# Kernel optimization log

Measured on AMD Instinct MI355X. Metric: run time of the kernel, lower is better.

The kernel has to match this reference:

```python
import jax, jax.numpy as jnp
import numpy as np

N, E, D_IN, H, L = 50000, 800000, 256, 128, 6


def setup_inputs() -> dict:
    key = jax.random.key(0)
    ks = jax.random.split(key, 16)
    s = 0.05
    return {
        "x": jax.random.normal(ks[0], (N, D_IN), jnp.float32),
        "edge_index": jax.random.randint(ks[1], (2, E), 0, N, jnp.int32),
        "y": jax.random.randint(ks[2], (N,), 0, L, jnp.int32),
        # input projection (stored [in, out])
        "lin_w": jax.random.normal(ks[3], (D_IN, H), jnp.float32) * s,
        "lin_b": jnp.zeros((H,), jnp.float32),
        # GatedGraphConv 1: message weight [H,H], GRUCell params (torch layout [3H,H])
        "w1": jax.random.normal(ks[4], (H, H), jnp.float32) * s,
        "wih1": jax.random.normal(ks[5], (3 * H, H), jnp.float32) * s,
        "whh1": jax.random.normal(ks[6], (3 * H, H), jnp.float32) * s,
        "bih1": jnp.zeros((3 * H,), jnp.float32),
        "bhh1": jnp.zeros((3 * H,), jnp.float32),
        # GatedGraphConv 2
        "w2": jax.random.normal(ks[7], (H, H), jnp.float32) * s,
        "wih2": jax.random.normal(ks[8], (3 * H, H), jnp.float32) * s,
        "whh2": jax.random.normal(ks[9], (3 * H, H), jnp.float32) * s,
        "bih2": jnp.zeros((3 * H,), jnp.float32),
        "bhh2": jnp.zeros((3 * H,), jnp.float32),
        # classifier
        "cls_w": jax.random.normal(ks[10], (H, L), jnp.float32) * s,
        "cls_b": jnp.zeros((L,), jnp.float32),
    }


def _gated_conv(h, src, dst, w, wih, whh, bih, bhh):
    # PyG GatedGraphConv, num_layers=1: m = h @ W; aggregate add src->dst; GRUCell(m_agg, h)
    m = h @ w                                   # [N,H]
    agg = jax.ops.segment_sum(m[src], dst, num_segments=N)  # scatter-add [N,H]
    gi = agg @ wih.T + bih                      # [N,3H]
    gh = h @ whh.T + bhh                        # [N,3H]
    i_r, i_z, i_n = jnp.split(gi, 3, axis=-1)
    h_r, h_z, h_n = jnp.split(gh, 3, axis=-1)
    r = jax.nn.sigmoid(i_r + h_r)
    z = jax.nn.sigmoid(i_z + h_z)
    n = jnp.tanh(i_n + r * h_n)
    return (1.0 - z) * n + z * h


def reference(x, edge_index, y, lin_w, lin_b, w1, wih1, whh1, bih1, bhh1,
              w2, wih2, whh2, bih2, bhh2, cls_w, cls_b):
    src, dst = edge_index[0], edge_index[1]
    h = x @ lin_w + lin_b                       # [N,H]
    h = _gated_conv(h, src, dst, w1, wih1, whh1, bih1, bhh1)
    h = jax.nn.elu(h)
    h = _gated_conv(h, src, dst, w2, wih2, whh2, bih2, bhh2)
    features = h
    output = h @ cls_w + cls_b                  # [N,L]
    logp = jax.nn.log_softmax(output, axis=-1)
    loss = -jnp.mean(jnp.take_along_axis(logp, y[:, None], axis=-1))
    return output, loss, features
```

## Files before the change

### kernel.cpp

```cpp
#include <hip/hip_runtime.h>
#include <cstddef>
#include <cstdint>

typedef __attribute__((ext_vector_type(8))) short bf16x8;
typedef __attribute__((ext_vector_type(4))) float f32x4;
typedef __attribute__((ext_vector_type(8))) unsigned short u16x8;

__device__ inline unsigned short f2bf(float f) {
    unsigned u = __builtin_bit_cast(unsigned, f);
    u += 0x7FFF + ((u >> 16) & 1);
    return (unsigned short)(u >> 16);
}
__device__ inline float bfbits_lo(unsigned v) { return __builtin_bit_cast(float, v << 16); }
__device__ inline float bfbits_hi(unsigned v) { return __builtin_bit_cast(float, v & 0xffff0000u); }
__device__ inline float bf2f(unsigned short b) { return __builtin_bit_cast(float, (unsigned)b << 16); }

__device__ inline float fsigmoid(float x) { return 1.0f / (1.0f + __expf(-x)); }
__device__ inline float ftanh(float x)    { return 1.0f - 2.0f / (__expf(2.0f * x) + 1.0f); }

__device__ inline int swzB(int row, int slot) {
    return row * 64 + ((slot ^ ((row >> 1) & 3)) << 4);
}
__device__ inline bf16x8 ldbf8(const unsigned short* p) {
    u16x8 v = *(const u16x8*)p;
    return __builtin_bit_cast(bf16x8, v);
}

__global__ __launch_bounds__(256)
void prepack_kernel(const float* __restrict__ S, unsigned short* __restrict__ P,
                    int K, int C, int trans)
{
    int idx = blockIdx.x * 256 + threadIdx.x;
    if (idx >= K * C) return;
    int kk = idx & 31;
    int c  = (idx >> 5) % C;
    int kc = idx / (32 * C);
    int k  = kc * 32 + kk;
    float v = trans ? S[(size_t)c * K + k] : S[(size_t)k * C + c];
    P[idx] = f2bf(v);
}

__global__ __launch_bounds__(256)
void wcomb_kernel(const float* __restrict__ Wm, const float* __restrict__ Wih,
                  unsigned short* __restrict__ P)
{
    int idx = blockIdx.x * 256 + threadIdx.x;
    int kk = idx & 31;
    int c  = (idx >> 5) % 384;
    int kc = idx / (32 * 384);
    int d  = kc * 32 + kk;
    const float4* a = (const float4*)&Wm[(size_t)d * 128];
    const float4* b = (const float4*)&Wih[(size_t)c * 128];
    float s = 0.0f;
#pragma unroll 8
    for (int t = 0; t < 32; ++t) {
        float4 av = a[t], bv = b[t];
        s += av.x * bv.x + av.y * bv.y + av.z * bv.z + av.w * bv.w;
    }
    P[idx] = f2bf(s);
}

template<int KC>
__global__ __launch_bounds__(256)
void mfma_xw(const float* __restrict__ A, const unsigned short* __restrict__ P,
             const float* __restrict__ bias, unsigned short* __restrict__ Cbf, int M)
{
    __shared__ unsigned short Ab[KC * 2048];
    const int tid  = threadIdx.x;
    const int l    = tid & 63;
    const int w    = tid >> 6;
    const int wr   = w >> 1, wc = w & 1;
    const int row0 = blockIdx.x * 64;
    const int K    = KC * 32;

    {
        int row = tid >> 2, slot = tid & 3, kpos = slot * 8;
#pragma unroll
        for (int kc = 0; kc < KC; ++kc) {
            unsigned short u[8];
            if (row0 + row < M) {
                const float* src = &A[(size_t)(row0 + row) * K + kc * 32 + kpos];
                float4 v0 = *(const float4*)src;
                float4 v1 = *(const float4*)(src + 4);
                u[0]=f2bf(v0.x); u[1]=f2bf(v0.y); u[2]=f2bf(v0.z); u[3]=f2bf(v0.w);
                u[4]=f2bf(v1.x); u[5]=f2bf(v1.y); u[6]=f2bf(v1.z); u[7]=f2bf(v1.w);
            } else {
#pragma unroll
                for (int q = 0; q < 8; ++q) u[q] = 0;
            }
            *(u16x8*)((char*)Ab + kc * 4096 + swzB(row, slot)) = *(u16x8*)u;
        }
    }
    __syncthreads();

    f32x4 acc[2][4];
#pragma unroll
    for (int i = 0; i < 2; ++i)
#pragma unroll
        for (int j = 0; j < 4; ++j) acc[i][j] = (f32x4){0.f, 0.f, 0.f, 0.f};

#pragma unroll
    for (int kc = 0; kc < KC; ++kc) {
        bf16x8 af[2], bf[4];
#pragma unroll
        for (int rt = 0; rt < 2; ++rt)
            af[rt] = *(const bf16x8*)((const char*)Ab + kc * 4096 +
                                      swzB(wr * 32 + rt * 16 + (l & 15), l >> 4));
#pragma unroll
        for (int ct = 0; ct < 4; ++ct) {
            int c = wc * 64 + ct * 16 + (l & 15);
            bf[ct] = ldbf8(&P[(size_t)kc * 4096 + c * 32 + (l >> 4) * 8]);
        }
#pragma unroll
        for (int rt = 0; rt < 2; ++rt)
#pragma unroll
            for (int ct = 0; ct < 4; ++ct)
                acc[rt][ct] = __builtin_amdgcn_mfma_f32_16x16x32_bf16(af[rt], bf[ct], acc[rt][ct], 0, 0, 0);
    }

#pragma unroll
    for (int rt = 0; rt < 2; ++rt)
#pragma unroll
        for (int ct = 0; ct < 4; ++ct) {
            int col = wc * 64 + ct * 16 + (l & 15);
            float bv = bias ? bias[col] : 0.0f;
#pragma unroll
            for (int j = 0; j < 4; ++j) {
                int row = row0 + wr * 32 + rt * 16 + (l >> 4) * 4 + j;
                if (row < M) Cbf[(size_t)row * 128 + col] = f2bf(acc[rt][ct][j] + bv);
            }
        }
}

template<int ELU, int OUTF32>
__global__ __launch_bounds__(512, 2)
void mfma_gru(const unsigned short* __restrict__ agghbf, const unsigned short* __restrict__ hbf,
              const unsigned short* __restrict__ wcP, const unsigned short* __restrict__ whhP,
              const float* __restrict__ bih, const float* __restrict__ bhh,
              float* __restrict__ hout, unsigned short* __restrict__ houtbf,
              int M, int ntiles)
{
    __shared__ unsigned short Aa[4096];
    __shared__ unsigned short Ah[4096];
    const int tid = threadIdx.x;
    const int l   = tid & 63;
    const int g   = tid >> 6;

    const int skc = tid >> 7;
    const int t3  = tid & 127;
    const int srow = t3 >> 2, sslot = t3 & 3, skpos = sslot * 8;
    const int slbyte = skc * 2048 + swzB(srow, sslot);

    const int unit = g * 16 + (l & 15);
    const int kcu = unit >> 5, slotu = (unit & 31) >> 3, elemu = unit & 7;
    const float bir = bih[unit], biz = bih[128 + unit], bin = bih[256 + unit];
    const float bhr = bhh[unit], bhz = bhh[128 + unit], bhn = bhh[256 + unit];

    bf16x8 BW[4][3], BU[4][3];
#pragma unroll
    for (int kc = 0; kc < 4; ++kc)
#pragma unroll
        for (int gr = 0; gr < 3; ++gr) {
            int c = gr * 128 + g * 16 + (l & 15);
            size_t boff = (size_t)kc * 12288 + c * 32 + (l >> 4) * 8;
            BW[kc][gr] = ldbf8(&wcP[boff]);
            BU[kc][gr] = ldbf8(&whhP[boff]);
        }

    u16x8 ua = (u16x8){0,0,0,0,0,0,0,0};
    u16x8 uh = (u16x8){0,0,0,0,0,0,0,0};
    {
        int row0 = blockIdx.x * 32;
        if (row0 + srow < M && row0 < ntiles * 32) {
            size_t goff = (size_t)(row0 + srow) * 128 + skc * 32 + skpos;
            ua = *(const u16x8*)&agghbf[goff];
            uh = *(const u16x8*)&hbf[goff];
        }
    }

    for (int t = blockIdx.x; t < ntiles; t += gridDim.x) {
        const int row0 = t * 32;
        __syncthreads();
        *(u16x8*)((char*)Aa + slbyte) = ua;
        *(u16x8*)((char*)Ah + slbyte) = uh;
        __syncthreads();

        {
            int tn = t + gridDim.x;
            ua = (u16x8){0,0,0,0,0,0,0,0};
            uh = (u16x8){0,0,0,0,0,0,0,0};
            if (tn < ntiles) {
                int r0n = tn * 32;
                if (r0n + srow < M) {
                    size_t goff = (size_t)(r0n + srow) * 128 + skc * 32 + skpos;
                    ua = *(const u16x8*)&agghbf[goff];
                    uh = *(const u16x8*)&hbf[goff];
                }
            }
        }

        f32x4 gi[3][2], gh[3][2];
#pragma unroll
        for (int gr = 0; gr < 3; ++gr)
#pragma unroll
            for (int rt = 0; rt < 2; ++rt) {
                gi[gr][rt] = (f32x4){0.f, 0.f, 0.f, 0.f};
                gh[gr][rt] = (f32x4){0.f, 0.f, 0.f, 0.f};
            }

#pragma unroll
        for (int kc = 0; kc < 4; ++kc) {
            bf16x8 aa[2], ah[2];
#pragma unroll
            for (int rt = 0; rt < 2; ++rt) {
                int lbyte = kc * 2048 + swzB(rt * 16 + (l & 15), l >> 4);
                aa[rt] = *(const bf16x8*)((const char*)Aa + lbyte);
                ah[rt] = *(const bf16x8*)((const char*)Ah + lbyte);
            }
#pragma unroll
            for (int gr = 0; gr < 3; ++gr)
#pragma unroll
                for (int rt = 0; rt < 2; ++rt) {
                    gi[gr][rt] = __builtin_amdgcn_mfma_f32_16x16x32_bf16(aa[rt], BW[kc][gr], gi[gr][rt], 0, 0, 0);
                    gh[gr][rt] = __builtin_amdgcn_mfma_f32_16x16x32_bf16(ah[rt], BU[kc][gr], gh[gr][rt], 0, 0, 0);
                }
        }

#pragma unroll
        for (int rt = 0; rt < 2; ++rt)
#pragma unroll
            for (int j = 0; j < 4; ++j) {
                int rl = rt * 16 + (l >> 4) * 4 + j;
                int row = row0 + rl;
                if (row >= M) continue;
                float hv = bf2f(*(const unsigned short*)
                                ((const char*)Ah + kcu * 2048 + swzB(rl, slotu) + elemu * 2));
                float rr = fsigmoid(gi[0][rt][j] + bir + gh[0][rt][j] + bhr);
                float z  = fsigmoid(gi[1][rt][j] + biz + gh[1][rt][j] + bhz);
                float nn = ftanh(gi[2][rt][j] + bin + rr * (gh[2][rt][j] + bhn));
                float o  = (1.0f - z) * nn + z * hv;
                if (ELU) o = (o > 0.0f) ? o : (__expf(o) - 1.0f);
                if (OUTF32) hout[(size_t)row * 128 + unit] = o;
                else        houtbf[(size_t)row * 128 + unit] = f2bf(o);
            }
    }
}


#define CHUNK 4096

__global__ __launch_bounds__(1024)
void chunk_hist_kernel(const int* __restrict__ dst, int* __restrict__ bh, int E)
{
    __shared__ int lh[256];
    const int c = blockIdx.x, tid = threadIdx.x;
    if (tid < 256) lh[tid] = 0;
    __syncthreads();
#pragma unroll
    for (int q = 0; q < 4; ++q) {
        int e = c * CHUNK + q * 1024 + tid;
        if (e < E) atomicAdd(&lh[dst[e] >> 8], 1);
    }
    __syncthreads();
    if (tid < 256) bh[c * 256 + tid] = lh[tid];
}

__global__ __launch_bounds__(256)
void matscan_kernel(int* __restrict__ bh, int* __restrict__ bcnt, int* __restrict__ bbase,
                    int* __restrict__ off, int NCH, int N, int E)
{
    __shared__ int wt[4];
    const int b = threadIdx.x, lane = b & 63, w4 = b >> 6;
    int running = 0;
    for (int c = 0; c < NCH; ++c) {
        int t = bh[c * 256 + b];
        bh[c * 256 + b] = running;
        running += t;
    }
    bcnt[b] = running;
    int v = running, s = v;
#pragma unroll
    for (int o = 1; o < 64; o <<= 1) {
        int n = __shfl_up(s, o, 64);
        if (lane >= o) s += n;
    }
    if (lane == 63) wt[w4] = s;
    __syncthreads();
    int wpre = 0;
    for (int q = 0; q < w4; ++q) wpre += wt[q];
    bbase[b] = wpre + s - v;
    if (b == 0) off[N] = E;
}

__global__ __launch_bounds__(1024)
void place_kernel(const int* __restrict__ src, const int* __restrict__ dst,
                  const int* __restrict__ bh, const int* __restrict__ bbase,
                  unsigned long long* __restrict__ bpair, int E)
{
    __shared__ int cur[256];
    const int c = blockIdx.x, tid = threadIdx.x;
    if (tid < 256) cur[tid] = bbase[tid] + bh[c * 256 + tid];
    __syncthreads();
#pragma unroll
    for (int q = 0; q < 4; ++q) {
        int e = c * CHUNK + q * 1024 + tid;
        if (e < E) {
            int d = dst[e];
            int pos = atomicAdd(&cur[d >> 8], 1);
            bpair[(size_t)pos] = ((unsigned long long)(unsigned)d << 32) | (unsigned)src[e];
        }
    }
}

__global__ __launch_bounds__(1024)
void bucket_sort_kernel(const unsigned long long* __restrict__ bpair,
                        const int* __restrict__ bcnt, const int* __restrict__ bbase,
                        int* __restrict__ off, int* __restrict__ ssrc, int N)
{
    __shared__ int hist[256];
    __shared__ int wt[4];
    const int b = blockIdx.x;
    const int tid = threadIdx.x;
    const int cnt = bcnt[b];
    const int base = bbase[b];

    if (tid < 256) hist[tid] = 0;
    __syncthreads();
    for (int i = tid; i < cnt; i += 1024) {
        unsigned long long p = bpair[(size_t)base + i];
        atomicAdd(&hist[(int)(p >> 32) & 255], 1);
    }
    __syncthreads();

    int ex = 0;
    {
        int lane = tid & 63, w4 = tid >> 6;
        int v = (tid < 256) ? hist[tid] : 0;
        int s = v;
#pragma unroll
        for (int o = 1; o < 64; o <<= 1) {
            int n = __shfl_up(s, o, 64);
            if (lane >= o) s += n;
        }
        if (tid < 256 && lane == 63) wt[w4] = s;
        __syncthreads();
        if (tid < 256) {
            int wpre = 0;
            for (int q = 0; q < w4; ++q) wpre += wt[q];
            ex = wpre + s - v;
        }
    }
    __syncthreads();
    if (tid < 256) {
        int d = (b << 8) + tid;
        if (d < N) off[d] = base + ex;
        hist[tid] = ex;
    }
    __syncthreads();
    for (int i = tid; i < cnt; i += 1024) {
        unsigned long long p = bpair[(size_t)base + i];
        int d = (int)(p >> 32) & 255;
        int pos = atomicAdd(&hist[d], 1);
        ssrc[(size_t)base + pos] = (int)(unsigned)p;
    }
}

__global__ __launch_bounds__(256)
void gather_agg_bf(const unsigned short* __restrict__ m, const int* __restrict__ off,
                   const int* __restrict__ ssrc, unsigned short* __restrict__ agg, int N)
{
    int w = (blockIdx.x * 256 + threadIdx.x) >> 6;
    int lane = threadIdx.x & 63;
    if (w >= N) return;
    int half = lane >> 5, hl = lane & 31;
    int e0 = off[w], e1 = off[w + 1];
    float a0[4] = {0.f, 0.f, 0.f, 0.f};
    float a1[4] = {0.f, 0.f, 0.f, 0.f};
    int e = e0 + half;
    for (; e + 2 < e1; e += 4) {
        int s0 = ssrc[e], s1 = ssrc[e + 2];
        uint2 v0 = *(const uint2*)&m[(size_t)s0 * 128 + hl * 4];
        uint2 v1 = *(const uint2*)&m[(size_t)s1 * 128 + hl * 4];
        a0[0] += bfbits_lo(v0.x); a0[1] += bfbits_hi(v0.x);
        a0[2] += bfbits_lo(v0.y); a0[3] += bfbits_hi(v0.y);
        a1[0] += bfbits_lo(v1.x); a1[1] += bfbits_hi(v1.x);
        a1[2] += bfbits_lo(v1.y); a1[3] += bfbits_hi(v1.y);
    }
    if (e < e1) {
        int s0 = ssrc[e];
        uint2 v0 = *(const uint2*)&m[(size_t)s0 * 128 + hl * 4];
        a0[0] += bfbits_lo(v0.x); a0[1] += bfbits_hi(v0.x);
        a0[2] += bfbits_lo(v0.y); a0[3] += bfbits_hi(v0.y);
    }
    float o[4];
#pragma unroll
    for (int j = 0; j < 4; ++j) o[j] = a0[j] + a1[j];
#pragma unroll
    for (int j = 0; j < 4; ++j) o[j] += __shfl_xor(o[j], 32, 64);
    if (half == 0) {
        uint2 pk;
        pk.x = (unsigned)f2bf(o[0]) | ((unsigned)f2bf(o[1]) << 16);
        pk.y = (unsigned)f2bf(o[2]) | ((unsigned)f2bf(o[3]) << 16);
        *(uint2*)&agg[(size_t)w * 128 + hl * 4] = pk;
    }
}

__global__ __launch_bounds__(256)
void cls_kernel(const float* __restrict__ h, const float* __restrict__ W,
                const float* __restrict__ b, const int* __restrict__ y,
                float* __restrict__ logitsOut, float* __restrict__ partials,
                int N, float invN)
{
    __shared__ float pl[4];
    const int wid  = threadIdx.x >> 6;
    const int lane = threadIdx.x & 63;
    const int gw   = blockIdx.x * 4 + wid;
    if (threadIdx.x < 4) pl[threadIdx.x] = 0.0f;
    __syncthreads();
    if (gw < N) {
        float h0 = h[(size_t)gw * 128 + lane * 2];
        float h1 = h[(size_t)gw * 128 + lane * 2 + 1];
        float acc[6];
#pragma unroll
        for (int c = 0; c < 6; ++c)
            acc[c] = h0 * W[(lane * 2) * 6 + c] + h1 * W[(lane * 2 + 1) * 6 + c];
#pragma unroll
        for (int off = 32; off >= 1; off >>= 1)
#pragma unroll
            for (int c = 0; c < 6; ++c)
                acc[c] += __shfl_xor(acc[c], off, 64);
        float logit[6];
#pragma unroll
        for (int c = 0; c < 6; ++c) logit[c] = acc[c] + b[c];
#pragma unroll
        for (int c = 0; c < 6; ++c)
            if (lane == c) logitsOut[(size_t)gw * 6 + c] = logit[c];
        if (lane == 0) {
            float mx = logit[0];
#pragma unroll
            for (int c = 1; c < 6; ++c) mx = fmaxf(mx, logit[c]);
            float se = 0.0f;
#pragma unroll
            for (int c = 0; c < 6; ++c) se += expf(logit[c] - mx);
            float lse = mx + logf(se);
            int yy = y[gw];
            float ly = 0.0f;
#pragma unroll
            for (int c = 0; c < 6; ++c)
                if (yy == c) ly = logit[c];
            pl[wid] = (lse - ly) * invN;
        }
    }
    __syncthreads();
    if (threadIdx.x == 0)
        partials[blockIdx.x] = pl[0] + pl[1] + pl[2] + pl[3];
}

__global__ __launch_bounds__(1024)
void loss_reduce(const float* __restrict__ partials, float* __restrict__ loss, int P)
{
    __shared__ float buf[1024];
    float s = 0.0f;
    for (int i = threadIdx.x; i < (unsigned)P; i += 1024) s += partials[i];
    buf[threadIdx.x] = s;
    __syncthreads();
    for (int o = 512; o >= 1; o >>= 1) {
        if (threadIdx.x < (unsigned)o) buf[threadIdx.x] += buf[threadIdx.x + o];
        __syncthreads();
    }
    if (threadIdx.x == 0) loss[0] = buf[0];
}

extern "C" void kernel_launch(void* const* d_in, const int* in_sizes, int n_in,
                              void* d_out, int out_size, void* d_ws, size_t ws_size,
                              hipStream_t stream)
{
    const float* x     = (const float*)d_in[0];
    const int*   eidx  = (const int*)d_in[1];
    const int*   y     = (const int*)d_in[2];
    const float* lin_w = (const float*)d_in[3];
    const float* lin_b = (const float*)d_in[4];
    const float* w1    = (const float*)d_in[5];
    const float* wih1  = (const float*)d_in[6];
    const float* whh1  = (const float*)d_in[7];
    const float* bih1  = (const float*)d_in[8];
    const float* bhh1  = (const float*)d_in[9];
    const float* w2    = (const float*)d_in[10];
    const float* wih2  = (const float*)d_in[11];
    const float* whh2  = (const float*)d_in[12];
    const float* bih2  = (const float*)d_in[13];
    const float* bhh2  = (const float*)d_in[14];
    const float* cls_w = (const float*)d_in[15];
    const float* cls_b = (const float*)d_in[16];

    const int N   = in_sizes[2];
    const int E   = in_sizes[1] / 2;
    const int L   = 6;
    const size_t NH = (size_t)N * 128;
    const int P   = (N + 3) / 4;
    const int NT  = (N + 31) / 32;
    const int NCH = (E + CHUNK - 1) / CHUNK;
    const int NBK = (N + 255) >> 8;

    float* out    = (float*)d_out;
    float* logits = out;
    float* loss   = out + (size_t)N * L;
    float* feats  = out + (size_t)N * L + 1;

    float* ws   = (float*)d_ws;
    float* part = ws;

    unsigned short* h_bf   = (unsigned short*)(part + P);
    unsigned short* aggh   = h_bf + NH;
    unsigned short* linP   = aggh + NH;
    unsigned short* wc1P   = linP  + 32768;
    unsigned short* whh1P  = wc1P  + 49152;
    unsigned short* wc2P   = whh1P + 49152;
    unsigned short* whh2P  = wc2P  + 49152;

    int* off   = (int*)(whh2P + 49152);
    int* bcnt  = off + (N + 2);
    int* bbase = bcnt + 256;
    int* bh    = bbase + 256;
    unsigned long long* bpair =
        (unsigned long long*)(((uintptr_t)(bh + (size_t)NCH * 256) + 7) & ~(uintptr_t)7);
    int* ssrc  = (int*)(bpair + E);

    const int* src = eidx;
    const int* dst = eidx + E;

    dim3 blk(256);
    unsigned ngridW = (unsigned)((N + 3) / 4);
    unsigned gemmG  = (unsigned)((N + 63) / 64);
    unsigned gruG   = (unsigned)(NT < 256 ? NT : 256);

    chunk_hist_kernel<<<dim3((unsigned)NCH), dim3(1024), 0, stream>>>(dst, bh, E);
    matscan_kernel<<<dim3(1), dim3(256), 0, stream>>>(bh, bcnt, bbase, off, NCH, N, E);
    place_kernel<<<dim3((unsigned)NCH), dim3(1024), 0, stream>>>(src, dst, bh, bbase, bpair, E);
    bucket_sort_kernel<<<dim3((unsigned)NBK), dim3(1024), 0, stream>>>(bpair, bcnt, bbase, off, ssrc, N);

    prepack_kernel<<<dim3(128), blk, 0, stream>>>(lin_w, linP, 256, 128, 0);
    wcomb_kernel<<<dim3(192), blk, 0, stream>>>(w1, wih1, wc1P);
    wcomb_kernel<<<dim3(192), blk, 0, stream>>>(w2, wih2, wc2P);
    prepack_kernel<<<dim3(192), blk, 0, stream>>>(whh1, whh1P, 128, 384, 1);
    prepack_kernel<<<dim3(192), blk, 0, stream>>>(whh2, whh2P, 128, 384, 1);

    mfma_xw<8><<<dim3(gemmG), blk, 0, stream>>>(x, linP, lin_b, h_bf, N);

    gather_agg_bf<<<dim3(ngridW), blk, 0, stream>>>(h_bf, off, ssrc, aggh, N);
    mfma_gru<1, 0><<<dim3(gruG), dim3(512), 0, stream>>>(aggh, h_bf, wc1P, whh1P, bih1, bhh1, nullptr, h_bf, N, NT);

    gather_agg_bf<<<dim3(ngridW), blk, 0, stream>>>(h_bf, off, ssrc, aggh, N);
    mfma_gru<0, 1><<<dim3(gruG), dim3(512), 0, stream>>>(aggh, h_bf, wc2P, whh2P, bih2, bhh2, feats, nullptr, N, NT);

    cls_kernel<<<dim3(ngridW), blk, 0, stream>>>(feats, cls_w, cls_b, y, logits, part, N, 1.0f / (float)N);
    loss_reduce<<<dim3(1), dim3(1024), 0, stream>>>(part, loss, P);
}
```

Baseline: 271.8 us.

## Parallelize chunk-histogram column scan across 256 blocks

New measurement: 228.9 us (median of 2 runs). 15.8% less time.

```diff
diff --git a/kernel.cpp b/kernel.cpp
--- a/kernel.cpp
+++ b/kernel.cpp
@@ -266,19 +266,44 @@
 }
 
 __global__ __launch_bounds__(256)
-void matscan_kernel(int* __restrict__ bh, int* __restrict__ bcnt, int* __restrict__ bbase,
-                    int* __restrict__ off, int NCH, int N, int E)
+void colscan_kernel(int* __restrict__ bh, int* __restrict__ bcnt, int NCH)
 {
     __shared__ int wt[4];
-    const int b = threadIdx.x, lane = b & 63, w4 = b >> 6;
-    int running = 0;
-    for (int c = 0; c < NCH; ++c) {
-        int t = bh[c * 256 + b];
-        bh[c * 256 + b] = running;
-        running += t;
-    }
-    bcnt[b] = running;
-    int v = running, s = v;
+    __shared__ int carry;
+    const int b = blockIdx.x;
+    const int tid = threadIdx.x, lane = tid & 63, w4 = tid >> 6;
+    if (tid == 0) carry = 0;
+    __syncthreads();
+    for (int base = 0; base < NCH; base += 256) {
+        int c = base + tid;
+        int v = (c < NCH) ? bh[c * 256 + b] : 0;
+        int s = v;
+#pragma unroll
+        for (int o = 1; o < 64; o <<= 1) {
+            int n = __shfl_up(s, o, 64);
+            if (lane >= o) s += n;
+        }
+        if (lane == 63) wt[w4] = s;
+        __syncthreads();
+        int wpre = 0;
+        for (int q = 0; q < w4; ++q) wpre += wt[q];
+        int ex = carry + wpre + s - v;
+        if (c < NCH) bh[c * 256 + b] = ex;
+        __syncthreads();
+        if (tid == 255) carry = ex + v;
+        __syncthreads();
+    }
+    if (tid == 0) bcnt[b] = carry;
+}
+
+__global__ __launch_bounds__(256)
+void bscan2_kernel(const int* __restrict__ bcnt, int* __restrict__ bbase,
+                   int* __restrict__ off, int N, int E)
+{
+    __shared__ int wt[4];
+    const int tid = threadIdx.x, lane = tid & 63, w4 = tid >> 6;
+    int v = bcnt[tid];
+    int s = v;
 #pragma unroll
     for (int o = 1; o < 64; o <<= 1) {
         int n = __shfl_up(s, o, 64);
@@ -288,8 +313,8 @@
     __syncthreads();
     int wpre = 0;
     for (int q = 0; q < w4; ++q) wpre += wt[q];
-    bbase[b] = wpre + s - v;
-    if (b == 0) off[N] = E;
+    bbase[tid] = wpre + s - v;
+    if (tid == 0) off[N] = E;
 }
 
 __global__ __launch_bounds__(1024)
@@ -535,7 +560,8 @@
     unsigned gruG   = (unsigned)(NT < 256 ? NT : 256);
 
     chunk_hist_kernel<<<dim3((unsigned)NCH), dim3(1024), 0, stream>>>(dst, bh, E);
-    matscan_kernel<<<dim3(1), dim3(256), 0, stream>>>(bh, bcnt, bbase, off, NCH, N, E);
+    colscan_kernel<<<dim3(256), dim3(256), 0, stream>>>(bh, bcnt, NCH);
+    bscan2_kernel<<<dim3(1), dim3(256), 0, stream>>>(bcnt, bbase, off, N, E);
     place_kernel<<<dim3((unsigned)NCH), dim3(1024), 0, stream>>>(src, dst, bh, bbase, bpair, E);
     bucket_sort_kernel<<<dim3((unsigned)NBK), dim3(1024), 0, stream>>>(bpair, bcnt, bbase, off, ssrc, N);
 
```
